# Kernel tuning notes

Hardware: AMD Instinct MI355X
Metric: run time of the kernel (lower is better)

## Reference

```python
import jax, jax.numpy as jnp
import numpy as np

D_MODEL = 1024
N_HEADS = 16
D_K = D_MODEL // N_HEADS
B, S = 2, 2048
NEG = -1.0e9


def setup_inputs() -> dict:
    key = jax.random.key(0)
    ks = jax.random.split(key, 12)
    sc = 1.0 / np.sqrt(D_MODEL)
    inp = {
        'query': jax.random.normal(ks[0], (B, S, D_MODEL), jnp.float32),
        'key': jax.random.normal(ks[1], (B, S, D_MODEL), jnp.float32),
        'value': jax.random.normal(ks[2], (B, S, D_MODEL), jnp.float32),
        # causal mask, broadcast over batch: 1 = attend, 0 = masked
        'mask': jnp.broadcast_to(jnp.tril(jnp.ones((S, S), jnp.int32)), (B, S, S)),
        'wq': jax.random.normal(ks[3], (D_MODEL, D_MODEL), jnp.float32) * sc,
        'bq': jnp.zeros((D_MODEL,), jnp.float32),
        'wk': jax.random.normal(ks[4], (D_MODEL, D_MODEL), jnp.float32) * sc,
        'bk': jnp.zeros((D_MODEL,), jnp.float32),
        'wv': jax.random.normal(ks[5], (D_MODEL, D_MODEL), jnp.float32) * sc,
        'bv': jnp.zeros((D_MODEL,), jnp.float32),
        'wo': jax.random.normal(ks[6], (D_MODEL, D_MODEL), jnp.float32) * sc,
        'bo': jnp.zeros((D_MODEL,), jnp.float32),
    }
    return inp


def reference(query, key, value, mask, wq, bq, wk, bk, wv, bv, wo, bo):
    b, sq, _ = query.shape
    sk = key.shape[1]
    # linear projections, split into heads: [B, H, S, d_k]
    def proj(x, w, bias, s):
        return (x @ w + bias).reshape(b, s, N_HEADS, D_K).transpose(0, 2, 1, 3)
    Q = proj(query, wq, bq, sq)
    K = proj(key, wk, bk, sk)
    V = proj(value, wv, bv, sk)
    # scaled dot-product attention with full score matrix [B, H, Sq, Sk]
    scores = jnp.einsum('bhqd,bhkd->bhqk', Q, K) / np.sqrt(D_K)
    scores = jnp.where(mask[:, None, :, :] == 0, NEG, scores)
    attn = jax.nn.softmax(scores, axis=-1)
    ctx = jnp.einsum('bhqk,bhkd->bhqd', attn, V)
    ctx = ctx.transpose(0, 2, 1, 3).reshape(b, sq, D_MODEL)
    return ctx @ wo + bo
```

## Files before the change

### kernel.cpp

```cpp
#include <hip/hip_runtime.h>
#include <stdint.h>

#define AS1 __attribute__((address_space(1)))
#define AS3 __attribute__((address_space(3)))

typedef __attribute__((ext_vector_type(8))) __bf16 bf16x8;
typedef __attribute__((ext_vector_type(4))) float f32x4;
typedef __attribute__((ext_vector_type(4))) unsigned int u32x4;
typedef __attribute__((ext_vector_type(2))) unsigned int u32x2;

static __device__ __forceinline__ void gload16(const void* g, void* l) {
    __builtin_amdgcn_global_load_lds((AS1 void*)(uintptr_t)g, (AS3 void*)l, 16, 0, 0);
}

static __device__ __forceinline__ unsigned cvt_pk_bf16(float lo, float hi) {
    unsigned r;
    asm volatile("v_cvt_pk_bf16_f32 %0, %1, %2" : "=v"(r) : "v"(lo), "v"(hi));
    return r;
}
static __device__ __forceinline__ unsigned short f2bf(float f) {
    return (unsigned short)(cvt_pk_bf16(f, 0.f) & 0xffffu);
}

static __device__ __forceinline__ f32x4 mfma16(bf16x8 a, bf16x8 b, f32x4 c) {
    return __builtin_amdgcn_mfma_f32_16x16x32_bf16(a, b, c, 0, 0, 0);
}

__global__ __launch_bounds__(256) void k_wtrans4(const float* __restrict__ w0,
                                                 const float* __restrict__ w1,
                                                 const float* __restrict__ w2,
                                                 const float* __restrict__ w3,
                                                 unsigned short* __restrict__ o0,
                                                 unsigned short* __restrict__ o1,
                                                 unsigned short* __restrict__ o2,
                                                 unsigned short* __restrict__ o3) {
    const float* W;
    unsigned short* Wt;
    switch (blockIdx.z) {
        case 0: W = w0; Wt = o0; break;
        case 1: W = w1; Wt = o1; break;
        case 2: W = w2; Wt = o2; break;
        default: W = w3; Wt = o3; break;
    }
    __shared__ unsigned short tile[64][72];
    const int tid = threadIdx.x;
    const int k0 = blockIdx.x * 64, n0 = blockIdx.y * 64;
#pragma unroll
    for (int j = 0; j < 4; ++j) {
        int c = j * 256 + tid;
        int kr = c >> 4, c4 = c & 15;
        f32x4 v = *(const f32x4*)(W + (size_t)(k0 + kr) * 1024 + n0 + c4 * 4);
#pragma unroll
        for (int e = 0; e < 4; ++e) tile[c4 * 4 + e][kr] = f2bf(v[e]);
    }
    __syncthreads();
#pragma unroll
    for (int j = 0; j < 2; ++j) {
        int c = j * 256 + tid;
        int nr = c >> 3, kc = c & 7;
        union { unsigned short s[8]; u32x4 v; } t;
#pragma unroll
        for (int e = 0; e < 8; ++e) t.s[e] = tile[nr][kc * 8 + e];
        *(u32x4*)(Wt + (size_t)(n0 + nr) * 1024 + k0 + kc * 8) = t.v;
    }
}

__global__ __launch_bounds__(256) void k_cvt3(const float* __restrict__ q,
                                              const float* __restrict__ k,
                                              const float* __restrict__ v,
                                              unsigned short* __restrict__ oq,
                                              unsigned short* __restrict__ ok,
                                              unsigned short* __restrict__ ov) {
    const float* src; unsigned short* dst;
    switch (blockIdx.z) {
        case 0: src = q; dst = oq; break;
        case 1: src = k; dst = ok; break;
        default: src = v; dst = ov; break;
    }
    const size_t i = ((size_t)blockIdx.x * 256 + threadIdx.x) * 8;
    f32x4 a = *(const f32x4*)(src + i);
    f32x4 b = *(const f32x4*)(src + i + 4);
    u32x4 o;
    o[0] = cvt_pk_bf16(a[0], a[1]);
    o[1] = cvt_pk_bf16(a[2], a[3]);
    o[2] = cvt_pk_bf16(b[0], b[1]);
    o[3] = cvt_pk_bf16(b[2], b[3]);
    *(u32x4*)(dst + i) = o;
}

template <int A_F32, int OUT_F32>
static __device__ __forceinline__ void gemm_body(const void* __restrict__ Ap,
                                                 const unsigned short* __restrict__ Bt,
                                                 const float* __restrict__ bias,
                                                 void* __restrict__ Cp,
                                                 int M, int N, int K, float cscale,
                                                 char* smem) {
    constexpr int ASZ = A_F32 ? 16384 : 8192;
    char* sA = smem;
    char* sB = smem + 2 * ASZ;
    const int tid = threadIdx.x;
    const int wave = tid >> 6, lane = tid & 63, g = lane >> 4, l16 = lane & 15;
    const int wm = wave & 1, wn = wave >> 1;
    const int m0 = blockIdx.x * 64, n0 = blockIdx.y * 128;

    f32x4 acc[2][4];
#pragma unroll
    for (int i = 0; i < 2; ++i)
#pragma unroll
        for (int j = 0; j < 4; ++j) acc[i][j] = (f32x4){0.f, 0.f, 0.f, 0.f};

    auto STAGE = [&](int k0, int buf) {
        if constexpr (A_F32) {
            const float* A = (const float*)Ap;
            char* dst = sA + buf * ASZ;
#pragma unroll
            for (int j = 0; j < 4; ++j) {
                int c = j * 256 + tid;
                int row = c >> 4, w = c & 15, kc = w ^ (row & 15);
                gload16(A + (size_t)(m0 + row) * K + k0 + kc * 4, dst + c * 16);
            }
        } else {
            const unsigned short* A = (const unsigned short*)Ap;
            char* dst = sA + buf * ASZ;
#pragma unroll
            for (int j = 0; j < 2; ++j) {
                int c = j * 256 + tid;
                int row = c >> 3, w = c & 7, kc = w ^ (row & 7);
                gload16(A + (size_t)(m0 + row) * K + k0 + kc * 8, dst + c * 16);
            }
        }
        char* dst = sB + buf * 16384;
#pragma unroll
        for (int j = 0; j < 4; ++j) {
            int c = j * 256 + tid;
            int row = c >> 3, w = c & 7, kc = w ^ (row & 7);
            gload16(Bt + (size_t)(n0 + row) * K + k0 + kc * 8, dst + c * 16);
        }
    };

    const int nkt = K >> 6;
    STAGE(0, 0);
    __syncthreads();
    int cur = 0;
#pragma unroll 1
    for (int kt = 0; kt < nkt; ++kt) {
        if (kt + 1 < nkt) STAGE((kt + 1) << 6, cur ^ 1);
        const char* sAc = sA + cur * ASZ;
        const char* sBc = sB + cur * 16384;
#pragma unroll
        for (int ks = 0; ks < 2; ++ks) {
            bf16x8 af[2];
#pragma unroll
            for (int mi = 0; mi < 2; ++mi) {
                int row = wm * 32 + mi * 16 + l16;
                if constexpr (A_F32) {
                    int c0 = (ks * 8 + g * 2) ^ (row & 15);
                    int c1 = (ks * 8 + g * 2 + 1) ^ (row & 15);
                    f32x4 lo = *(const f32x4*)(sAc + row * 256 + c0 * 16);
                    f32x4 hi = *(const f32x4*)(sAc + row * 256 + c1 * 16);
                    union { unsigned u[4]; bf16x8 v; } cv;
                    cv.u[0] = cvt_pk_bf16(lo[0], lo[1]);
                    cv.u[1] = cvt_pk_bf16(lo[2], lo[3]);
                    cv.u[2] = cvt_pk_bf16(hi[0], hi[1]);
                    cv.u[3] = cvt_pk_bf16(hi[2], hi[3]);
                    af[mi] = cv.v;
                } else {
                    int c = (ks * 4 + g) ^ (row & 7);
                    af[mi] = *(const bf16x8*)(sAc + row * 128 + c * 16);
                }
            }
#pragma unroll
            for (int ni = 0; ni < 4; ++ni) {
                int row = wn * 64 + ni * 16 + l16;
                int c = (ks * 4 + g) ^ (row & 7);
                bf16x8 bfr = *(const bf16x8*)(sBc + row * 128 + c * 16);
#pragma unroll
                for (int mi = 0; mi < 2; ++mi)
                    acc[mi][ni] = mfma16(af[mi], bfr, acc[mi][ni]);
            }
        }
        __syncthreads();
        cur ^= 1;
    }
#pragma unroll
    for (int ni = 0; ni < 4; ++ni) {
        int col = n0 + wn * 64 + ni * 16 + l16;
        float bn = bias[col];
#pragma unroll
        for (int mi = 0; mi < 2; ++mi) {
            int rbase = m0 + wm * 32 + mi * 16 + g * 4;
#pragma unroll
            for (int r = 0; r < 4; ++r) {
                float v = (acc[mi][ni][r] + bn) * cscale;
                if constexpr (OUT_F32)
                    ((float*)Cp)[(size_t)(rbase + r) * N + col] = v;
                else
                    ((unsigned short*)Cp)[(size_t)(rbase + r) * N + col] = f2bf(v);
            }
        }
    }
}

__global__ __launch_bounds__(256) void k_gemm_qkv(
    const unsigned short* __restrict__ Aq, const unsigned short* __restrict__ Ak,
    const unsigned short* __restrict__ Av,
    const unsigned short* __restrict__ Wq, const unsigned short* __restrict__ Wk,
    const unsigned short* __restrict__ Wv,
    const float* __restrict__ bq, const float* __restrict__ bk, const float* __restrict__ bv,
    unsigned short* __restrict__ Q2, unsigned short* __restrict__ K2,
    unsigned short* __restrict__ V2) {
    extern __shared__ __align__(16) char smem[];
    const unsigned short* A; const unsigned short* Bt; const float* bias;
    unsigned short* C; float sc;
    switch (blockIdx.z) {
        case 0:  A = Aq; Bt = Wq; bias = bq; C = Q2; sc = 0.18033688011112042f; break;
        case 1:  A = Ak; Bt = Wk; bias = bk; C = K2; sc = 1.0f; break;
        default: A = Av; Bt = Wv; bias = bv; C = V2; sc = 1.0f; break;
    }
    gemm_body<0, 0>(A, Bt, bias, C, 4096, 1024, 1024, sc, smem);
}

__global__ __launch_bounds__(256) void k_gemm_o(const unsigned short* __restrict__ ctx,
                                                const unsigned short* __restrict__ Wo,
                                                const float* __restrict__ bo,
                                                float* __restrict__ out) {
    extern __shared__ __align__(16) char smem[];
    gemm_body<0, 1>(ctx, Wo, bo, out, 4096, 1024, 1024, 1.0f, smem);
}

__global__ __launch_bounds__(256) void k_vtrans(const unsigned short* __restrict__ V2,
                                                unsigned short* __restrict__ Vt) {
    __shared__ unsigned short tile[64][72];
    const int tid = threadIdx.x;
    const int s0 = blockIdx.x * 64;
    const int bh = blockIdx.y, b = bh >> 4, h = bh & 15;
#pragma unroll
    for (int j = 0; j < 2; ++j) {
        int c = j * 256 + tid;
        int sr = c >> 3, dc = c & 7;
        union { u32x4 v; unsigned short s[8]; } t;
        t.v = *(const u32x4*)(V2 + (size_t)(b * 2048 + s0 + sr) * 1024 + h * 64 + dc * 8);
#pragma unroll
        for (int e = 0; e < 8; ++e) tile[dc * 8 + e][sr] = t.s[e];
    }
    __syncthreads();
#pragma unroll
    for (int j = 0; j < 2; ++j) {
        int c = j * 256 + tid;
        int dr = c >> 3, sc = c & 7;
        union { unsigned short s[8]; u32x4 v; } t;
#pragma unroll
        for (int e = 0; e < 8; ++e) t.s[e] = tile[dr][sc * 8 + e];
        *(u32x4*)(Vt + ((size_t)bh * 64 + dr) * 2048 + s0 + sc * 8) = t.v;
    }
}

__global__ __launch_bounds__(128) void k_attn(const unsigned short* __restrict__ Q2,
                                              const unsigned short* __restrict__ K2,
                                              const unsigned short* __restrict__ Vt,
                                              unsigned short* __restrict__ ctx) {
    __shared__ __align__(16) char sK[8192];
    __shared__ __align__(16) char sV[2][8192];
    __shared__ __align__(16) char sP[2][2048];

    const int tid = threadIdx.x, w = tid >> 6, lane = tid & 63;
    const int g = lane >> 4, l16 = lane & 15;
    const int bid = blockIdx.x;
    const int xcd = bid & 7, j = bid >> 3;
    const int bh = xcd * 4 + (j & 3);
    const int p = j >> 2;
    const int b = bh >> 4, h = bh & 15;
    const int swzl = (l16 & 7) << 4;

    const int r0 = tid >> 3;
    const int sc0 = (tid & 7) ^ (r0 & 7);
    const unsigned short* ksrc = K2 + (size_t)(b * 2048 + r0) * 1024 + h * 64 + sc0 * 8;
    const unsigned short* vsrc = Vt + ((size_t)bh * 64 + r0) * 2048 + sc0 * 8;
    char* const myp = sP[w];

#pragma unroll 1
    for (int t2 = 0; t2 < 2; ++t2) {
        const int t = t2 ? p : (63 - p);
        const int wq0 = t * 32 + w * 16;
        const int qg = wq0 + l16;

        const unsigned short* qp = Q2 + (size_t)(b * 2048 + wq0 + l16) * 1024 + h * 64;
        bf16x8 qf0 = *(const bf16x8*)(qp + g * 8);
        bf16x8 qf1 = *(const bf16x8*)(qp + 32 + g * 8);

        f32x4 accO[4];
#pragma unroll
        for (int i = 0; i < 4; ++i) accO[i] = (f32x4){0.f, 0.f, 0.f, 0.f};
        float m = 0.f, lsum = 0.f;

        const int nkv = (t >> 1) + 1;
        const int diag = t >> 1;
        __syncthreads();
#pragma unroll
        for (int rr = 0; rr < 4; ++rr) {
            gload16(ksrc + (size_t)(rr * 16) * 1024, sK + rr * 2048 + tid * 16);
            gload16(vsrc + (size_t)(rr * 16) * 2048, sV[0] + rr * 2048 + tid * 16);
        }
        __syncthreads();

#pragma unroll 1
        for (int kt = 0; kt < nkv; ++kt) {
            const int cur = kt & 1;
            const int kv0 = kt * 64;
            float s[16];
            __builtin_amdgcn_s_setprio(1);
#pragma unroll
            for (int blk = 0; blk < 4; ++blk) {
                const int rl = blk * 16 + l16;
                const char* krow = sK + rl * 128;
                bf16x8 kf0 = *(const bf16x8*)(krow + ((g << 4) ^ swzl));
                bf16x8 kf1 = *(const bf16x8*)(krow + (((4 + g) << 4) ^ swzl));
                f32x4 a = (f32x4){0.f, 0.f, 0.f, 0.f};
                a = mfma16(kf0, qf0, a);
                a = mfma16(kf1, qf1, a);
#pragma unroll
                for (int rr = 0; rr < 4; ++rr) s[blk * 4 + rr] = a[rr];
            }
            __builtin_amdgcn_s_setprio(0);
            __syncthreads();
            if (kt + 1 < nkv) {
#pragma unroll
                for (int rr = 0; rr < 4; ++rr) {
                    gload16(ksrc + (size_t)(kv0 + 64 + rr * 16) * 1024, sK + rr * 2048 + tid * 16);
                    gload16(vsrc + (size_t)(rr * 16) * 2048 + (kv0 + 64), sV[cur ^ 1] + rr * 2048 + tid * 16);
                }
            }
            if (kt == diag) {
#pragma unroll
                for (int j2 = 0; j2 < 16; ++j2) {
                    int kvg = kv0 + (j2 >> 2) * 16 + g * 4 + (j2 & 3);
                    if (kvg > qg) s[j2] = -1e9f;
                }
            }
            float ps = 0.f;
            unsigned pk[8];
#pragma unroll
            for (int j2 = 0; j2 < 8; ++j2) {
                float p0 = __builtin_exp2f(s[2 * j2] - m);
                float p1 = __builtin_exp2f(s[2 * j2 + 1] - m);
                ps += p0 + p1;
                pk[j2] = cvt_pk_bf16(p0, p1);
            }
            if (__any(ps > 16777216.f)) {
                float c1 = fmaxf(fmaxf(s[0], s[1]), s[2]);
                c1 = fmaxf(fmaxf(c1, s[3]), s[4]);
                c1 = fmaxf(fmaxf(c1, s[5]), s[6]);
                c1 = fmaxf(c1, s[7]);
                float c2 = fmaxf(fmaxf(s[8], s[9]), s[10]);
                c2 = fmaxf(fmaxf(c2, s[11]), s[12]);
                c2 = fmaxf(fmaxf(c2, s[13]), s[14]);
                c2 = fmaxf(c2, s[15]);
                float mx = fmaxf(c1, c2);
                mx = fmaxf(mx, __shfl_xor(mx, 16));
                mx = fmaxf(mx, __shfl_xor(mx, 32));
                float mnew = fmaxf(m, mx);
                float scl = __builtin_exp2f(m - mnew);
                lsum *= scl;
#pragma unroll
                for (int dt = 0; dt < 4; ++dt) accO[dt] = accO[dt] * scl;
                m = mnew;
                ps = 0.f;
#pragma unroll
                for (int j2 = 0; j2 < 8; ++j2) {
                    float p0 = __builtin_exp2f(s[2 * j2] - m);
                    float p1 = __builtin_exp2f(s[2 * j2 + 1] - m);
                    ps += p0 + p1;
                    pk[j2] = cvt_pk_bf16(p0, p1);
                }
            }
            lsum += ps;
#pragma unroll
            for (int blk = 0; blk < 4; ++blk) {
                u32x2 pw = {pk[blk * 2], pk[blk * 2 + 1]};
                *(u32x2*)(myp + l16 * 128 + ((blk * 32 + g * 8) ^ swzl)) = pw;
            }
            __builtin_amdgcn_s_setprio(1);
#pragma unroll
            for (int kvh = 0; kvh < 2; ++kvh) {
                bf16x8 pf = *(const bf16x8*)(myp + l16 * 128 + ((kvh * 64 + g * 16) ^ swzl));
#pragma unroll
                for (int dt = 0; dt < 4; ++dt) {
                    const int rv = dt * 16 + l16;
                    bf16x8 vf = *(const bf16x8*)(sV[cur] + rv * 128 + (((kvh * 4 + g) << 4) ^ swzl));
                    accO[dt] = mfma16(vf, pf, accO[dt]);
                }
            }
            __builtin_amdgcn_s_setprio(0);
            __syncthreads();
        }
        float v = lsum;
        v += __shfl_xor(v, 16);
        v += __shfl_xor(v, 32);
        float inv = 1.f / v;
        unsigned short* cp = ctx + (size_t)(b * 2048 + wq0 + l16) * 1024 + h * 64 + g * 4;
#pragma unroll
        for (int dt = 0; dt < 4; ++dt) {
            u32x2 o;
            o[0] = cvt_pk_bf16(accO[dt][0] * inv, accO[dt][1] * inv);
            o[1] = cvt_pk_bf16(accO[dt][2] * inv, accO[dt][3] * inv);
            *(u32x2*)(cp + dt * 16) = o;
        }
    }
}

extern "C" void kernel_launch(void* const* d_in, const int* in_sizes, int n_in,
                              void* d_out, int out_size, void* d_ws, size_t ws_size,
                              hipStream_t stream) {
    const float* query = (const float*)d_in[0];
    const float* key   = (const float*)d_in[1];
    const float* value = (const float*)d_in[2];
    const float* wq = (const float*)d_in[4];
    const float* bq = (const float*)d_in[5];
    const float* wk = (const float*)d_in[6];
    const float* bk = (const float*)d_in[7];
    const float* wv = (const float*)d_in[8];
    const float* bv = (const float*)d_in[9];
    const float* wo = (const float*)d_in[10];
    const float* bo = (const float*)d_in[11];
    float* out = (float*)d_out;

    char* ws = (char*)d_ws;
    unsigned short* Wtq = (unsigned short*)ws;
    unsigned short* Wtk = Wtq + 1024 * 1024;
    unsigned short* Wtv = Wtk + 1024 * 1024;
    unsigned short* Wto = Wtv + 1024 * 1024;
    unsigned short* Q2  = Wto + 1024 * 1024;
    unsigned short* K2  = Q2 + 4096 * 1024;
    unsigned short* V2  = K2 + 4096 * 1024;
    unsigned short* Aq  = V2 + 4096 * 1024;
    unsigned short* Ak  = Aq + 4096 * 1024;
    unsigned short* Av  = Ak + 4096 * 1024;
    unsigned short* Vt  = Aq;
    unsigned short* ctx = Ak;

    dim3 blk(256);
    k_wtrans4<<<dim3(16, 16, 4), blk, 0, stream>>>(wq, wk, wv, wo, Wtq, Wtk, Wtv, Wto);
    k_cvt3<<<dim3(2048, 1, 3), blk, 0, stream>>>(query, key, value, Aq, Ak, Av);

    k_gemm_qkv<<<dim3(64, 8, 3), blk, 49152, stream>>>(Aq, Ak, Av,
                                                       Wtq, Wtk, Wtv, bq, bk, bv,
                                                       Q2, K2, V2);

    k_vtrans<<<dim3(32, 32), blk, 0, stream>>>(V2, Vt);
    k_attn<<<dim3(1024), dim3(128), 0, stream>>>(Q2, K2, Vt, ctx);

    k_gemm_o<<<dim3(64, 8), blk, 49152, stream>>>(ctx, Wto, bo, out);
}
```

Measured before the change: 119.5 us.

## Rewrite attention kernel with 32x32 MFMA, register-resident P, and 128-row query tiles

```diff
diff --git a/kernel.cpp b/kernel.cpp
--- a/kernel.cpp
+++ b/kernel.cpp
@@ -6,6 +6,7 @@
 
 typedef __attribute__((ext_vector_type(8))) __bf16 bf16x8;
 typedef __attribute__((ext_vector_type(4))) float f32x4;
+typedef __attribute__((ext_vector_type(16))) float f32x16;
 typedef __attribute__((ext_vector_type(4))) unsigned int u32x4;
 typedef __attribute__((ext_vector_type(2))) unsigned int u32x2;
 
@@ -24,6 +25,17 @@
 
 static __device__ __forceinline__ f32x4 mfma16(bf16x8 a, bf16x8 b, f32x4 c) {
     return __builtin_amdgcn_mfma_f32_16x16x32_bf16(a, b, c, 0, 0, 0);
+}
+static __device__ __forceinline__ f32x16 mfma32(bf16x8 a, bf16x8 b, f32x16 c) {
+    return __builtin_amdgcn_mfma_f32_32x32x16_bf16(a, b, c, 0, 0, 0);
+}
+
+static __device__ __forceinline__ float fexp2(float x) {
+    return __builtin_amdgcn_exp2f(x);
+}
+
+static __device__ __forceinline__ void plane32_swap(unsigned& a, unsigned& b) {
+    asm volatile("v_permlane32_swap_b32 %0, %1" : "+v"(a), "+v"(b));
 }
 
 __global__ __launch_bounds__(256) void k_wtrans4(const float* __restrict__ w0,
@@ -255,155 +267,166 @@
     }
 }
 
-__global__ __launch_bounds__(128) void k_attn(const unsigned short* __restrict__ Q2,
+__global__ __launch_bounds__(256) void k_attn(const unsigned short* __restrict__ Q2,
                                               const unsigned short* __restrict__ K2,
                                               const unsigned short* __restrict__ Vt,
                                               unsigned short* __restrict__ ctx) {
-    __shared__ __align__(16) char sK[8192];
+    __shared__ __align__(16) char sK[2][8192];
     __shared__ __align__(16) char sV[2][8192];
-    __shared__ __align__(16) char sP[2][2048];
 
     const int tid = threadIdx.x, w = tid >> 6, lane = tid & 63;
-    const int g = lane >> 4, l16 = lane & 15;
+    const int l31 = lane & 31, hi = lane >> 5;
     const int bid = blockIdx.x;
     const int xcd = bid & 7, j = bid >> 3;
     const int bh = xcd * 4 + (j & 3);
     const int p = j >> 2;
     const int b = bh >> 4, h = bh & 15;
-    const int swzl = (l16 & 7) << 4;
-
-    const int r0 = tid >> 3;
-    const int sc0 = (tid & 7) ^ (r0 & 7);
-    const unsigned short* ksrc = K2 + (size_t)(b * 2048 + r0) * 1024 + h * 64 + sc0 * 8;
-    const unsigned short* vsrc = Vt + ((size_t)bh * 64 + r0) * 2048 + sc0 * 8;
-    char* const myp = sP[w];
+    const int swz = (l31 & 7) << 4;
+
+    const int row0 = tid >> 3, ch = tid & 7;
+    const int sc0 = ch ^ (row0 & 7);
+    const unsigned short* ksrc = K2 + (size_t)(b * 2048 + row0) * 1024 + h * 64 + sc0 * 8;
+    const unsigned short* vsrc = Vt + ((size_t)bh * 64 + row0) * 2048 + sc0 * 8;
 
 #pragma unroll 1
     for (int t2 = 0; t2 < 2; ++t2) {
-        const int t = t2 ? p : (63 - p);
-        const int wq0 = t * 32 + w * 16;
-        const int qg = wq0 + l16;
-
-        const unsigned short* qp = Q2 + (size_t)(b * 2048 + wq0 + l16) * 1024 + h * 64;
-        bf16x8 qf0 = *(const bf16x8*)(qp + g * 8);
-        bf16x8 qf1 = *(const bf16x8*)(qp + 32 + g * 8);
-
-        f32x4 accO[4];
-#pragma unroll
-        for (int i = 0; i < 4; ++i) accO[i] = (f32x4){0.f, 0.f, 0.f, 0.f};
+        const int T = t2 ? p : (15 - p);
+        const int wq0 = T * 128 + w * 32;
+        const int qg = wq0 + l31;
+
+        const unsigned short* qp = Q2 + (size_t)(b * 2048 + wq0 + l31) * 1024 + h * 64 + hi * 8;
+        bf16x8 qf[4];
+#pragma unroll
+        for (int kblk = 0; kblk < 4; ++kblk)
+            qf[kblk] = *(const bf16x8*)(qp + kblk * 16);
+
+        f32x16 accO0 = (f32x16)(0.f), accO1 = (f32x16)(0.f);
         float m = 0.f, lsum = 0.f;
 
-        const int nkv = (t >> 1) + 1;
-        const int diag = t >> 1;
-        __syncthreads();
-#pragma unroll
-        for (int rr = 0; rr < 4; ++rr) {
-            gload16(ksrc + (size_t)(rr * 16) * 1024, sK + rr * 2048 + tid * 16);
-            gload16(vsrc + (size_t)(rr * 16) * 2048, sV[0] + rr * 2048 + tid * 16);
-        }
+        const int nkv = 2 * T + 2;
+        const unsigned short* kst = ksrc;
+        const unsigned short* vst = vsrc;
+#pragma unroll
+        for (int rr = 0; rr < 2; ++rr) {
+            gload16(kst + (size_t)(rr * 32) * 1024, sK[0] + rr * 4096 + tid * 16);
+            gload16(vst + (size_t)(rr * 32) * 2048, sV[0] + rr * 4096 + tid * 16);
+        }
+        kst += 64 * 1024;
+        vst += 64;
         __syncthreads();
 
 #pragma unroll 1
         for (int kt = 0; kt < nkv; ++kt) {
             const int cur = kt & 1;
             const int kv0 = kt * 64;
-            float s[16];
+            if (kt + 1 < nkv) {
+#pragma unroll
+                for (int rr = 0; rr < 2; ++rr) {
+                    gload16(kst + (size_t)(rr * 32) * 1024, sK[cur ^ 1] + rr * 4096 + tid * 16);
+                    gload16(vst + (size_t)(rr * 32) * 2048, sV[cur ^ 1] + rr * 4096 + tid * 16);
+                }
+                kst += 64 * 1024;
+                vst += 64;
+            }
+            const char* kb = sK[cur];
+            const char* vb = sV[cur];
+            f32x16 s0v = (f32x16)(0.f), s1v = (f32x16)(0.f);
             __builtin_amdgcn_s_setprio(1);
 #pragma unroll
-            for (int blk = 0; blk < 4; ++blk) {
-                const int rl = blk * 16 + l16;
-                const char* krow = sK + rl * 128;
-                bf16x8 kf0 = *(const bf16x8*)(krow + ((g << 4) ^ swzl));
-                bf16x8 kf1 = *(const bf16x8*)(krow + (((4 + g) << 4) ^ swzl));
-                f32x4 a = (f32x4){0.f, 0.f, 0.f, 0.f};
-                a = mfma16(kf0, qf0, a);
-                a = mfma16(kf1, qf1, a);
-#pragma unroll
-                for (int rr = 0; rr < 4; ++rr) s[blk * 4 + rr] = a[rr];
-            }
+            for (int kblk = 0; kblk < 4; ++kblk) {
+                const int col = (kblk * 32 + hi * 16) ^ swz;
+                bf16x8 kf0 = *(const bf16x8*)(kb + l31 * 128 + col);
+                bf16x8 kf1 = *(const bf16x8*)(kb + (32 + l31) * 128 + col);
+                s0v = mfma32(kf0, qf[kblk], s0v);
+                s1v = mfma32(kf1, qf[kblk], s1v);
+            }
+            __builtin_amdgcn_s_setprio(0);
+            if (kv0 + 63 > wq0) {
+#pragma unroll
+                for (int r = 0; r < 16; ++r) {
+                    const int kvo = (r & 3) + 8 * (r >> 2) + 4 * hi;
+                    if (kv0 + kvo > qg) s0v[r] = -1e9f;
+                    if (kv0 + 32 + kvo > qg) s1v[r] = -1e9f;
+                }
+            }
+            float pa = 0.f, pb = 0.f, pc = 0.f, pd = 0.f;
+#pragma unroll
+            for (int r = 0; r < 4; ++r) {
+                s0v[4 * r + 0] = fexp2(s0v[4 * r + 0] - m);
+                s0v[4 * r + 1] = fexp2(s0v[4 * r + 1] - m);
+                s0v[4 * r + 2] = fexp2(s0v[4 * r + 2] - m);
+                s0v[4 * r + 3] = fexp2(s0v[4 * r + 3] - m);
+                s1v[4 * r + 0] = fexp2(s1v[4 * r + 0] - m);
+                s1v[4 * r + 1] = fexp2(s1v[4 * r + 1] - m);
+                s1v[4 * r + 2] = fexp2(s1v[4 * r + 2] - m);
+                s1v[4 * r + 3] = fexp2(s1v[4 * r + 3] - m);
+                pa += s0v[4 * r + 0] + s0v[4 * r + 1];
+                pb += s0v[4 * r + 2] + s0v[4 * r + 3];
+                pc += s1v[4 * r + 0] + s1v[4 * r + 1];
+                pd += s1v[4 * r + 2] + s1v[4 * r + 3];
+            }
+            float ps = (pa + pb) + (pc + pd);
+            if (__any(ps > 8388608.f)) {
+                const float scl = 0x1p-24f;
+                m += 24.f;
+                lsum *= scl;
+                ps *= scl;
+#pragma unroll
+                for (int r = 0; r < 16; ++r) {
+                    s0v[r] *= scl;
+                    s1v[r] *= scl;
+                    accO0[r] *= scl;
+                    accO1[r] *= scl;
+                }
+            }
+            lsum += ps;
+            __builtin_amdgcn_s_setprio(1);
+#define PV_K16(SV, KVBYTE)                                                     \
+            {                                                                  \
+                unsigned a0 = cvt_pk_bf16(SV[0], SV[1]);                       \
+                unsigned a1 = cvt_pk_bf16(SV[2], SV[3]);                       \
+                unsigned b0 = cvt_pk_bf16(SV[4], SV[5]);                       \
+                unsigned b1 = cvt_pk_bf16(SV[6], SV[7]);                       \
+                plane32_swap(a0, b0);                                          \
+                plane32_swap(a1, b1);                                          \
+                union { unsigned u[4]; bf16x8 v; } pfu;                        \
+                pfu.u[0] = a0; pfu.u[1] = a1; pfu.u[2] = b0; pfu.u[3] = b1;    \
+                const int col = ((KVBYTE) + hi * 16) ^ swz;                    \
+                bf16x8 vf0 = *(const bf16x8*)(vb + l31 * 128 + col);           \
+                bf16x8 vf1 = *(const bf16x8*)(vb + (32 + l31) * 128 + col);    \
+                accO0 = mfma32(vf0, pfu.v, accO0);                             \
+                accO1 = mfma32(vf1, pfu.v, accO1);                             \
+            }
+            {
+                float q0[8], q1[8], q2[8], q3[8];
+#pragma unroll
+                for (int i = 0; i < 8; ++i) {
+                    q0[i] = s0v[i];
+                    q1[i] = s0v[8 + i];
+                    q2[i] = s1v[i];
+                    q3[i] = s1v[8 + i];
+                }
+                PV_K16(q0, 0)
+                PV_K16(q1, 32)
+                PV_K16(q2, 64)
+                PV_K16(q3, 96)
+            }
+#undef PV_K16
             __builtin_amdgcn_s_setprio(0);
             __syncthreads();
-            if (kt + 1 < nkv) {
-#pragma unroll
-                for (int rr = 0; rr < 4; ++rr) {
-                    gload16(ksrc + (size_t)(kv0 + 64 + rr * 16) * 1024, sK + rr * 2048 + tid * 16);
-                    gload16(vsrc + (size_t)(rr * 16) * 2048 + (kv0 + 64), sV[cur ^ 1] + rr * 2048 + tid * 16);
-                }
-            }
-            if (kt == diag) {
-#pragma unroll
-                for (int j2 = 0; j2 < 16; ++j2) {
-                    int kvg = kv0 + (j2 >> 2) * 16 + g * 4 + (j2 & 3);
-                    if (kvg > qg) s[j2] = -1e9f;
-                }
-            }
-            float ps = 0.f;
-            unsigned pk[8];
-#pragma unroll
-            for (int j2 = 0; j2 < 8; ++j2) {
-                float p0 = __builtin_exp2f(s[2 * j2] - m);
-                float p1 = __builtin_exp2f(s[2 * j2 + 1] - m);
-                ps += p0 + p1;
-                pk[j2] = cvt_pk_bf16(p0, p1);
-            }
-            if (__any(ps > 16777216.f)) {
-                float c1 = fmaxf(fmaxf(s[0], s[1]), s[2]);
-                c1 = fmaxf(fmaxf(c1, s[3]), s[4]);
-                c1 = fmaxf(fmaxf(c1, s[5]), s[6]);
-                c1 = fmaxf(c1, s[7]);
-                float c2 = fmaxf(fmaxf(s[8], s[9]), s[10]);
-                c2 = fmaxf(fmaxf(c2, s[11]), s[12]);
-                c2 = fmaxf(fmaxf(c2, s[13]), s[14]);
-                c2 = fmaxf(c2, s[15]);
-                float mx = fmaxf(c1, c2);
-                mx = fmaxf(mx, __shfl_xor(mx, 16));
-                mx = fmaxf(mx, __shfl_xor(mx, 32));
-                float mnew = fmaxf(m, mx);
-                float scl = __builtin_exp2f(m - mnew);
-                lsum *= scl;
-#pragma unroll
-                for (int dt = 0; dt < 4; ++dt) accO[dt] = accO[dt] * scl;
-                m = mnew;
-                ps = 0.f;
-#pragma unroll
-                for (int j2 = 0; j2 < 8; ++j2) {
-                    float p0 = __builtin_exp2f(s[2 * j2] - m);
-                    float p1 = __builtin_exp2f(s[2 * j2 + 1] - m);
-                    ps += p0 + p1;
-                    pk[j2] = cvt_pk_bf16(p0, p1);
-                }
-            }
-            lsum += ps;
-#pragma unroll
-            for (int blk = 0; blk < 4; ++blk) {
-                u32x2 pw = {pk[blk * 2], pk[blk * 2 + 1]};
-                *(u32x2*)(myp + l16 * 128 + ((blk * 32 + g * 8) ^ swzl)) = pw;
-            }
-            __builtin_amdgcn_s_setprio(1);
-#pragma unroll
-            for (int kvh = 0; kvh < 2; ++kvh) {
-                bf16x8 pf = *(const bf16x8*)(myp + l16 * 128 + ((kvh * 64 + g * 16) ^ swzl));
-#pragma unroll
-                for (int dt = 0; dt < 4; ++dt) {
-                    const int rv = dt * 16 + l16;
-                    bf16x8 vf = *(const bf16x8*)(sV[cur] + rv * 128 + (((kvh * 4 + g) << 4) ^ swzl));
-                    accO[dt] = mfma16(vf, pf, accO[dt]);
-                }
-            }
-            __builtin_amdgcn_s_setprio(0);
-            __syncthreads();
-        }
-        float v = lsum;
-        v += __shfl_xor(v, 16);
-        v += __shfl_xor(v, 32);
-        float inv = 1.f / v;
-        unsigned short* cp = ctx + (size_t)(b * 2048 + wq0 + l16) * 1024 + h * 64 + g * 4;
-#pragma unroll
-        for (int dt = 0; dt < 4; ++dt) {
-            u32x2 o;
-            o[0] = cvt_pk_bf16(accO[dt][0] * inv, accO[dt][1] * inv);
-            o[1] = cvt_pk_bf16(accO[dt][2] * inv, accO[dt][3] * inv);
-            *(u32x2*)(cp + dt * 16) = o;
+        }
+        float vtot = lsum + __shfl_xor(lsum, 32);
+        float inv = 1.f / vtot;
+        unsigned short* cp = ctx + (size_t)(b * 2048 + wq0 + l31) * 1024 + h * 64 + hi * 4;
+#pragma unroll
+        for (int rq = 0; rq < 4; ++rq) {
+            u32x2 o0, o1;
+            o0[0] = cvt_pk_bf16(accO0[rq * 4 + 0] * inv, accO0[rq * 4 + 1] * inv);
+            o0[1] = cvt_pk_bf16(accO0[rq * 4 + 2] * inv, accO0[rq * 4 + 3] * inv);
+            o1[0] = cvt_pk_bf16(accO1[rq * 4 + 0] * inv, accO1[rq * 4 + 1] * inv);
+            o1[1] = cvt_pk_bf16(accO1[rq * 4 + 2] * inv, accO1[rq * 4 + 3] * inv);
+            *(u32x2*)(cp + rq * 8) = o0;
+            *(u32x2*)(cp + 32 + rq * 8) = o1;
         }
     }
 }
@@ -447,7 +470,7 @@
                                                        Q2, K2, V2);
 
     k_vtrans<<<dim3(32, 32), blk, 0, stream>>>(V2, Vt);
-    k_attn<<<dim3(1024), dim3(128), 0, stream>>>(Q2, K2, Vt, ctx);
+    k_attn<<<dim3(256), blk, 0, stream>>>(Q2, K2, Vt, ctx);
 
     k_gemm_o<<<dim3(64, 8), blk, 49152, stream>>>(ctx, Wto, bo, out);
 }
```

Result: slower. 125.9 us (+5.4%).
